# Kernel optimization log

Measured on AMD Instinct MI355X. Metric: run time of the kernel, lower is better.

Reference implementation:

```python
import jax, jax.numpy as jnp
import numpy as np

CONF_THRESH = 0.25


def setup_inputs() -> dict:
    key = jax.random.key(0)
    # Raw YOLO head output: [batch, n_anchors, 4 box + 1 objectness + 80 classes]
    output = jax.random.uniform(key, (16, 25200, 85), dtype=jnp.float32)
    return {"output": output}


def reference(output):
    # Faithful JAX version of ModelWrapper._process_raw_output fallback path.
    # Torch emits a variable-length [M, 6] tensor; with static shapes we emit
    # the dense [B, N, 6] decoded boxes with below-threshold rows zeroed
    # (equivalent information: masked rows are exactly the dropped ones).
    box_xy = output[..., 0:2]            # [B, N, 2]
    box_wh = output[..., 2:4]            # [B, N, 2]
    box_conf = output[..., 4]            # [B, N]
    box_cls = output[..., 5:]            # [B, N, C]

    half_wh = box_wh * 0.5
    xy_min = box_xy - half_wh            # xmin, ymin
    xy_max = box_xy + half_wh            # xmax, ymax

    max_scores = jnp.max(box_cls, axis=-1)                    # [B, N]
    max_cls_idx = jnp.argmax(box_cls, axis=-1)                # [B, N]
    scores = box_conf * max_scores                            # [B, N]
    mask = scores > CONF_THRESH                               # [B, N]

    boxes = jnp.concatenate(
        [xy_min, xy_max, scores[..., None],
         max_cls_idx.astype(output.dtype)[..., None]], axis=-1)  # [B, N, 6]
    return jnp.where(mask[..., None], boxes, jnp.zeros((), dtype=output.dtype))
```

## Files before the change

kernel.cpp:

```cpp
#include <hip/hip_runtime.h>

#define ROWS_PER_BLOCK 64
#define THREADS 64
#define ROW_F 85
#define NCLS 80
#define CONF_THRESH 0.25f

#define TILE_F (ROWS_PER_BLOCK * ROW_F)
#define TILE_V (TILE_F / 4)
#define PER_THREAD 21
#define TAIL_V (TILE_V - PER_THREAD * THREADS)

__global__ __launch_bounds__(THREADS) void yolo_post_kernel(
    const float* __restrict__ in, float* __restrict__ out, int nrows) {
  __shared__ float tile[TILE_F];

  const long long row0 = (long long)blockIdx.x * ROWS_PER_BLOCK;
  const long long base_f = row0 * ROW_F;
  const long long total_f = (long long)nrows * ROW_F;

  const float4* __restrict__ src = (const float4*)(in + base_f);
  float4* dstv = (float4*)tile;
  const int t = threadIdx.x;

  if (base_f + TILE_F <= total_f) {
    float4 v[PER_THREAD];
#pragma unroll
    for (int k = 0; k < PER_THREAD; ++k) {
      v[k] = src[t + k * THREADS];
    }
    float4 extra;
    if (t < TAIL_V) {
      extra = src[PER_THREAD * THREADS + t];
    }
#pragma unroll
    for (int k = 0; k < PER_THREAD; ++k) {
      dstv[t + k * THREADS] = v[k];
    }
    if (t < TAIL_V) {
      dstv[PER_THREAD * THREADS + t] = extra;
    }
  } else {
    for (int i = t; i < TILE_V; i += THREADS) {
      if (base_f + (long long)i * 4 + 3 < total_f) dstv[i] = src[i];
    }
  }
  __syncthreads();

  const long long r = row0 + t;
  if (r >= nrows) return;
  const float* row = tile + t * ROW_F;

  float cx = row[0];
  float cy = row[1];
  float hw = row[2] * 0.5f;
  float hh = row[3] * 0.5f;
  float conf = row[4];

  float best = row[5];
  int bidx = 0;
#pragma unroll
  for (int c = 1; c < NCLS; ++c) {
    float v = row[5 + c];
    bool gt = v > best;
    best = gt ? v : best;
    bidx = gt ? c : bidx;
  }

  float score = conf * best;
  bool keep = score > CONF_THRESH;

  float o0 = keep ? cx - hw : 0.0f;
  float o1 = keep ? cy - hh : 0.0f;
  float o2 = keep ? cx + hw : 0.0f;
  float o3 = keep ? cy + hh : 0.0f;
  float o4 = keep ? score : 0.0f;
  float o5 = keep ? (float)bidx : 0.0f;

  float* op = out + r * 6;
  op[0] = o0;
  op[1] = o1;
  op[2] = o2;
  op[3] = o3;
  op[4] = o4;
  op[5] = o5;
}

extern "C" void kernel_launch(void* const* d_in, const int* in_sizes, int n_in,
                              void* d_out, int out_size, void* d_ws, size_t ws_size,
                              hipStream_t stream) {
  const float* in = (const float*)d_in[0];
  float* out = (float*)d_out;
  const int nrows = in_sizes[0] / ROW_F;
  const int grid = (nrows + ROWS_PER_BLOCK - 1) / ROWS_PER_BLOCK;
  yolo_post_kernel<<<grid, THREADS, 0, stream>>>(in, out, nrows);
}
```

Measured before the change: 195.0 us.

## Split class argmax across two lanes per row and halve rows per block

Each row's 80-class argmax is now split between a pair of lanes, 40 classes each, and combined with a shuffle that keeps first-max tie semantics. Rows per block drop from 64 to 32, so the grid doubles and the shared tile halves. Each lane writes three of the six outputs. The intent is to shorten the serial compare chain per thread and raise occupancy and block count on a memory-bound kernel. The cost is extra shuffles and twice as many blocks each staging a smaller tile.

```diff
diff --git a/kernel.cpp b/kernel.cpp
--- a/kernel.cpp
+++ b/kernel.cpp
@@ -1,14 +1,15 @@
 #include <hip/hip_runtime.h>
 
-#define ROWS_PER_BLOCK 64
+#define ROWS_PER_BLOCK 32
 #define THREADS 64
 #define ROW_F 85
 #define NCLS 80
+#define HALF_CLS 40
 #define CONF_THRESH 0.25f
 
 #define TILE_F (ROWS_PER_BLOCK * ROW_F)
 #define TILE_V (TILE_F / 4)
-#define PER_THREAD 21
+#define PER_THREAD 10
 #define TAIL_V (TILE_V - PER_THREAD * THREADS)
 
 __global__ __launch_bounds__(THREADS) void yolo_post_kernel(
@@ -47,9 +48,12 @@
   }
   __syncthreads();
 
-  const long long r = row0 + t;
+  const int p = t >> 1;
+  const int j = t & 1;
+  const long long r = row0 + p;
   if (r >= nrows) return;
-  const float* row = tile + t * ROW_F;
+
+  const float* row = tile + p * ROW_F;
 
   float cx = row[0];
   float cy = row[1];
@@ -57,17 +61,30 @@
   float hh = row[3] * 0.5f;
   float conf = row[4];
 
-  float best = row[5];
+  const float* cls = row + 5 + j * HALF_CLS;
+  float best = cls[0];
   int bidx = 0;
 #pragma unroll
-  for (int c = 1; c < NCLS; ++c) {
-    float v = row[5 + c];
+  for (int c = 1; c < HALF_CLS; ++c) {
+    float v = cls[c];
     bool gt = v > best;
     best = gt ? v : best;
     bidx = gt ? c : bidx;
   }
 
-  float score = conf * best;
+  float obest = __shfl_xor(best, 1);
+  int oidx = __shfl_xor(bidx, 1);
+
+  float bl = j ? obest : best;
+  int   il = j ? oidx  : bidx;
+  float bh = j ? best  : obest;
+  int   ih = j ? bidx  : oidx;
+
+  bool hi = bh > bl;
+  float bestAll = hi ? bh : bl;
+  int idxAll = hi ? ih + HALF_CLS : il;
+
+  float score = conf * bestAll;
   bool keep = score > CONF_THRESH;
 
   float o0 = keep ? cx - hw : 0.0f;
@@ -75,15 +92,12 @@
   float o2 = keep ? cx + hw : 0.0f;
   float o3 = keep ? cy + hh : 0.0f;
   float o4 = keep ? score : 0.0f;
-  float o5 = keep ? (float)bidx : 0.0f;
+  float o5 = keep ? (float)idxAll : 0.0f;
 
-  float* op = out + r * 6;
-  op[0] = o0;
-  op[1] = o1;
-  op[2] = o2;
-  op[3] = o3;
-  op[4] = o4;
-  op[5] = o5;
+  float* op = out + r * 6 + j * 3;
+  op[0] = j ? o3 : o0;
+  op[1] = j ? o4 : o1;
+  op[2] = j ? o5 : o2;
 }
 
 extern "C" void kernel_launch(void* const* d_in, const int* in_sizes, int n_in,
```

After: 193.0 us. About the same (-1.0%).
